# Kernel optimization log

Hardware: AMD Instinct MI355X
Metric: run time of the kernel (lower is better)

Reference implementation:

```python
import jax, jax.numpy as jnp
import numpy as np

B, K, IN_DIM, H, D = 8, 4096, 512, 8, 64  # batch, tokens, in_dim, heads, per-head dim


def setup_inputs() -> dict:
    key = jax.random.key(0)
    ks = jax.random.split(key, 8)
    s = 0.02
    return {
        "x": jax.random.normal(ks[0], (B, K, IN_DIM), jnp.float32),
        "y": jax.random.normal(ks[1], (B, K, IN_DIM), jnp.float32),
        "Wq": jax.random.normal(ks[2], (IN_DIM, H * D), jnp.float32) * s,
        "bq": jnp.zeros((H * D,), jnp.float32),
        "Wk": jax.random.normal(ks[3], (IN_DIM, H * D), jnp.float32) * s,
        "bk": jnp.zeros((H * D,), jnp.float32),
        "Wv": jax.random.normal(ks[4], (IN_DIM, H * D), jnp.float32) * s,
        "bv": jnp.zeros((H * D,), jnp.float32),
        "Wp": jax.random.normal(ks[5], (IN_DIM, D), jnp.float32) * s,
        "gamma": jax.random.uniform(ks[6], (H, 1, 1, 1), jnp.float32) + 0.001,
    }


def _heads(t):
    # (B, K, H*D) -> (H, B, K, D); matches split_cat(t, D, dim=2, cat dim=0) head-major layout
    b, k, _ = t.shape
    return t.reshape(b, k, H, D).transpose(2, 0, 1, 3)


def reference(x, y, Wq, bq, Wk, bk, Wv, bv, Wp, gamma):
    q = _heads(x @ Wq + bq)   # (H,B,K,D)
    kk = _heads(x @ Wk + bk)  # (H,B,K,D)
    v = _heads(y @ Wv + bv)   # (H,B,K,D)
    # energy = q^T k contracted over tokens -> (H,B,D,D)
    energy = jnp.einsum('hbkd,hbke->hbde', q, kk)
    attn = jax.nn.softmax(energy, axis=-1)
    # out = v @ attn^T : out[k,q] = sum_e v[k,e] * attn[q,e]
    out = jnp.einsum('hbke,hbqe->hbkq', v, attn)  # (H,B,K,D)
    yp = y @ Wp  # projection(y): (B,K,D)
    out = (gamma * out + yp[None]) / (1.0 + gamma)
    return out.transpose(1, 0, 2, 3)  # (B,H,K,D)
```

## Files before the change

### kernel.cpp

```cpp
#include <hip/hip_runtime.h>

#define B_ 8
#define K_ 4096
#define IN_ 512
#define H_ 8
#define D_ 64
#define HD_ 512

typedef short bf16x8 __attribute__((ext_vector_type(8)));
typedef float f32x4 __attribute__((ext_vector_type(4)));
typedef unsigned short u16;
typedef unsigned short us8v __attribute__((ext_vector_type(8)));
typedef unsigned short us4v __attribute__((ext_vector_type(4)));

__device__ inline u16 f2bf_rn(float f) {
  unsigned u = __float_as_uint(f);
  u += 0x7fffu + ((u >> 16) & 1u);
  return (u16)(u >> 16);
}
__device__ inline float bf2f(u16 h) {
  return __uint_as_float(((unsigned)h) << 16);
}

__device__ inline void gl_lds16(const u16* g, u16* l) {
  __builtin_amdgcn_global_load_lds(
      (const __attribute__((address_space(1))) unsigned int*)g,
      (__attribute__((address_space(3))) unsigned int*)l, 16, 0, 0);
}


__global__ __launch_bounds__(256) void k_cvt_x(const float* __restrict__ x,
                                               u16* __restrict__ xt_hi,
                                               u16* __restrict__ xt_lo,
                                               float* __restrict__ svec) {
  const int kt = blockIdx.x, ct = blockIdx.y, b = blockIdx.z;
  __shared__ float Xs[64][65];
  const int tid = threadIdx.x;
  const float* src = x + ((size_t)b * K_ + kt * 64) * IN_ + ct * 64;
#pragma unroll
  for (int r = 0; r < 4; ++r) {
    int idx = tid + 256 * r;
    int k = idx >> 4, c4 = (idx & 15) * 4;
    f32x4 v = *(const f32x4*)(src + (size_t)k * IN_ + c4);
    Xs[k][c4 + 0] = v[0];
    Xs[k][c4 + 1] = v[1];
    Xs[k][c4 + 2] = v[2];
    Xs[k][c4 + 3] = v[3];
  }
  __syncthreads();
  if (tid < 64) {
    float s = 0.f;
#pragma unroll
    for (int k = 0; k < 64; ++k) s += Xs[k][tid];
    atomicAdd(&svec[b * IN_ + ct * 64 + tid], s);
  }
#pragma unroll
  for (int r = 0; r < 2; ++r) {
    int idx = tid + 256 * r;
    int c = idx >> 3, ck = (idx & 7) * 8;
    us8v hv, lv;
#pragma unroll
    for (int j = 0; j < 8; ++j) {
      float f = Xs[ck + j][c];
      u16 h = f2bf_rn(f);
      float lo = f - bf2f(h);
      hv[j] = h;
      lv[j] = f2bf_rn(lo);
    }
    size_t off = ((size_t)(b * IN_ + ct * 64 + c)) * K_ + kt * 64 + ck;
    *(us8v*)(xt_hi + off) = hv;
    *(us8v*)(xt_lo + off) = lv;
  }
}

__global__ __launch_bounds__(256) void k_cvt_y(const float* __restrict__ y,
                                               u16* __restrict__ yb) {
  size_t i = ((size_t)blockIdx.x * 256 + threadIdx.x) * 8;
  f32x4 v0 = *(const f32x4*)(y + i);
  f32x4 v1 = *(const f32x4*)(y + i + 4);
  us8v o;
  o[0] = f2bf_rn(v0[0]); o[1] = f2bf_rn(v0[1]);
  o[2] = f2bf_rn(v0[2]); o[3] = f2bf_rn(v0[3]);
  o[4] = f2bf_rn(v1[0]); o[5] = f2bf_rn(v1[1]);
  o[6] = f2bf_rn(v1[2]); o[7] = f2bf_rn(v1[3]);
  *(us8v*)(yb + i) = o;
}

__global__ __launch_bounds__(256) void k_cvt_w(
    const float* __restrict__ Wq, const float* __restrict__ Wk,
    u16* __restrict__ Wqt_hi, u16* __restrict__ Wqt_lo,
    u16* __restrict__ Wkt_hi, u16* __restrict__ Wkt_lo) {
  const int ti = blockIdx.x, tj = blockIdx.y;
  const float* src = blockIdx.z ? Wk : Wq;
  u16* dhi = blockIdx.z ? Wkt_hi : Wqt_hi;
  u16* dlo = blockIdx.z ? Wkt_lo : Wqt_lo;
  __shared__ float T[64][65];
  const int tid = threadIdx.x;
#pragma unroll
  for (int r = 0; r < 4; ++r) {
    int idx = tid + 256 * r;
    int rr = idx >> 4, c4 = (idx & 15) * 4;
    f32x4 v = *(const f32x4*)(src + (size_t)(tj * 64 + rr) * 512 + ti * 64 + c4);
    T[rr][c4 + 0] = v[0]; T[rr][c4 + 1] = v[1];
    T[rr][c4 + 2] = v[2]; T[rr][c4 + 3] = v[3];
  }
  __syncthreads();
#pragma unroll
  for (int r = 0; r < 2; ++r) {
    int idx = tid + 256 * r;
    int d = idx >> 3, ck = (idx & 7) * 8;
    us8v hv, lv;
#pragma unroll
    for (int j = 0; j < 8; ++j) {
      float f = T[ck + j][d];
      u16 h = f2bf_rn(f);
      hv[j] = h;
      lv[j] = f2bf_rn(f - bf2f(h));
    }
    size_t off = (size_t)(ti * 64 + d) * 512 + tj * 64 + ck;
    *(us8v*)(dhi + off) = hv;
    *(us8v*)(dlo + off) = lv;
  }
}

#define GP 72

__global__ __launch_bounds__(256, 2) void k_gram_mfma(
    const u16* __restrict__ xt_hi, const u16* __restrict__ xt_lo,
    float* __restrict__ G) {
  const int fid = blockIdx.x;
  const int kc = fid & 7;
  const int slot = fid >> 3;
  const int b = slot / 10;
  int pp = slot - b * 10, ti = 0;
  while (pp >= 4 - ti) { pp -= 4 - ti; ++ti; }
  const int tj = ti + pp;
  const bool diag = (ti == tj);
  __shared__ u16 P[4 * 128 * 64];
  u16* Pih = P;
  u16* Pil = P + 128 * 64;
  u16* Pjh = P + 2 * 128 * 64;
  u16* Pjl = P + 3 * 128 * 64;
  const int tid = threadIdx.x;
  const int wave = tid >> 6, lane = tid & 63;
  const int wm = wave & 1, wn = wave >> 1;
  const int m16 = lane & 15, quad = lane >> 4;
  const size_t base_i = ((size_t)(b * IN_ + ti * 128)) * K_;
  const size_t base_j = ((size_t)(b * IN_ + tj * 128)) * K_;
  const int lrow = lane >> 3;
  const int lcol = ((lane & 7) * 8) ^ (lrow << 3);
  const size_t loff = (size_t)lrow * K_ + lcol;
  const u16* PBh = diag ? Pih : Pjh;
  const u16* PBl = diag ? Pil : Pjl;

  f32x4 zf = {0.f, 0.f, 0.f, 0.f};
  f32x4 acc[4][4];
#pragma unroll
  for (int mt = 0; mt < 4; ++mt)
#pragma unroll
    for (int nt = 0; nt < 4; ++nt) acc[mt][nt] = zf;
  const int kbeg = kc * 512, kend = kbeg + 512;

  for (int k0 = kbeg; k0 < kend; k0 += 64) {
    __syncthreads();
#pragma unroll
    for (int r = 0; r < 4; ++r) {
      int rg = wave * 4 + r;
      size_t go = (size_t)(rg * 8) * K_ + k0 + loff;
      int lo = rg * 8 * 64;
      gl_lds16(xt_hi + base_i + go, &Pih[lo]);
      gl_lds16(xt_lo + base_i + go, &Pil[lo]);
      if (!diag) {
        gl_lds16(xt_hi + base_j + go, &Pjh[lo]);
        gl_lds16(xt_lo + base_j + go, &Pjl[lo]);
      }
    }
    __syncthreads();
#pragma unroll
    for (int kk = 0; kk < 64; kk += 32) {
      const int ac = (kk + quad * 8) ^ ((m16 & 7) << 3);
      bf16x8 ah[4], al[4], bh[4], bl[4];
#pragma unroll
      for (int t = 0; t < 4; ++t) {
        int ar = (wm * 64 + t * 16 + m16) * 64 + ac;
        ah[t] = *(const bf16x8*)&Pih[ar];
        al[t] = *(const bf16x8*)&Pil[ar];
        int br = (wn * 64 + t * 16 + m16) * 64 + ac;
        bh[t] = *(const bf16x8*)&PBh[br];
        bl[t] = *(const bf16x8*)&PBl[br];
      }
#pragma unroll
      for (int mt = 0; mt < 4; ++mt)
#pragma unroll
        for (int nt = 0; nt < 4; ++nt) {
          acc[mt][nt] = __builtin_amdgcn_mfma_f32_16x16x32_bf16(
              ah[mt], bh[nt], acc[mt][nt], 0, 0, 0);
          acc[mt][nt] = __builtin_amdgcn_mfma_f32_16x16x32_bf16(
              ah[mt], bl[nt], acc[mt][nt], 0, 0, 0);
          acc[mt][nt] = __builtin_amdgcn_mfma_f32_16x16x32_bf16(
              al[mt], bh[nt], acc[mt][nt], 0, 0, 0);
        }
    }
  }
  float* Gb = G + (size_t)b * IN_ * IN_;
#pragma unroll
  for (int mt = 0; mt < 4; ++mt)
#pragma unroll
    for (int nt = 0; nt < 4; ++nt)
#pragma unroll
      for (int r = 0; r < 4; ++r) {
        int gi = ti * 128 + wm * 64 + mt * 16 + quad * 4 + r;
        int gj = tj * 128 + wn * 64 + nt * 16 + m16;
        atomicAdd(&Gb[(size_t)gi * IN_ + gj], acc[mt][nt][r]);
      }
}

__global__ __launch_bounds__(256) void k_cvt_g(const float* __restrict__ G,
                                               u16* __restrict__ Ghi,
                                               u16* __restrict__ Glo) {
  const int ti = blockIdx.x, tj = blockIdx.y, b = blockIdx.z;
  if (tj < ti) return;
  const float* Gb = G + (size_t)b * IN_ * IN_;
  u16* ghb = Ghi + (size_t)b * IN_ * IN_;
  u16* glb = Glo + (size_t)b * IN_ * IN_;
  __shared__ float T[64][65];
  const int tid = threadIdx.x;
#pragma unroll
  for (int r = 0; r < 4; ++r) {
    int idx = tid + 256 * r;
    int rr = idx >> 4, c4 = (idx & 15) * 4;
    f32x4 v = *(const f32x4*)(Gb + (size_t)(ti * 64 + rr) * IN_ + tj * 64 + c4);
    T[rr][c4 + 0] = v[0]; T[rr][c4 + 1] = v[1];
    T[rr][c4 + 2] = v[2]; T[rr][c4 + 3] = v[3];
  }
  __syncthreads();
#pragma unroll
  for (int r = 0; r < 2; ++r) {
    int idx = tid + 256 * r;
    int rr = idx >> 3, ck = (idx & 7) * 8;
    us8v hv, lv;
#pragma unroll
    for (int j = 0; j < 8; ++j) {
      float f = T[rr][ck + j];
      u16 h = f2bf_rn(f);
      hv[j] = h;
      lv[j] = f2bf_rn(f - bf2f(h));
    }
    size_t off = (size_t)(ti * 64 + rr) * IN_ + tj * 64 + ck;
    *(us8v*)(ghb + off) = hv;
    *(us8v*)(glb + off) = lv;
  }
  if (ti != tj) {
#pragma unroll
    for (int r = 0; r < 2; ++r) {
      int idx = tid + 256 * r;
      int rr = idx >> 3, ck = (idx & 7) * 8;
      us8v hv, lv;
#pragma unroll
      for (int j = 0; j < 8; ++j) {
        float f = T[ck + j][rr];
        u16 h = f2bf_rn(f);
        hv[j] = h;
        lv[j] = f2bf_rn(f - bf2f(h));
      }
      size_t off = (size_t)(tj * 64 + rr) * IN_ + ti * 64 + ck;
      *(us8v*)(ghb + off) = hv;
      *(us8v*)(glb + off) = lv;
    }
  }
}

__global__ __launch_bounds__(256) void k_aall_mfma(
    const u16* __restrict__ Wqt_hi, const u16* __restrict__ Wqt_lo,
    const u16* __restrict__ Ghi, const u16* __restrict__ Glo,
    u16* __restrict__ Ahi, u16* __restrict__ Alo) {
  const int ct = blockIdx.x;
  const int hb = blockIdx.y;
  const int h = hb >> 3, b = hb & 7;
  __shared__ u16 S[4 * 64 * 64];
  u16* Ah = S;
  u16* Al = S + 64 * 64;
  u16* Bh = S + 2 * 64 * 64;
  u16* Bl = S + 3 * 64 * 64;
  const int tid = threadIdx.x;
  const int wave = tid >> 6, lane = tid & 63;
  const int m16 = lane & 15, quad = lane >> 4;
  const u16* Abase_h = Wqt_hi + (size_t)(h * 64) * IN_;
  const u16* Abase_l = Wqt_lo + (size_t)(h * 64) * IN_;
  const u16* Bbase_h = Ghi + (size_t)b * IN_ * IN_ + (size_t)(ct * 64) * IN_;
  const u16* Bbase_l = Glo + (size_t)b * IN_ * IN_ + (size_t)(ct * 64) * IN_;
  const int lrow = lane >> 3;
  const int lcol = ((lane & 7) * 8) ^ (lrow << 3);
  const size_t loff = (size_t)lrow * IN_ + lcol;
  f32x4 zf = {0.f, 0.f, 0.f, 0.f};
  f32x4 acc[4] = {zf, zf, zf, zf};
  for (int k0 = 0; k0 < IN_; k0 += 64) {
    __syncthreads();
#pragma unroll
    for (int r = 0; r < 2; ++r) {
      int rg = wave * 2 + r;
      size_t go = (size_t)(rg * 8) * IN_ + k0 + loff;
      int lo = rg * 8 * 64;
      gl_lds16(Abase_h + go, &Ah[lo]);
      gl_lds16(Abase_l + go, &Al[lo]);
      gl_lds16(Bbase_h + go, &Bh[lo]);
      gl_lds16(Bbase_l + go, &Bl[lo]);
    }
    __syncthreads();
#pragma unroll
    for (int kk = 0; kk < 64; kk += 32) {
      const int ac = (kk + quad * 8) ^ ((m16 & 7) << 3);
      int arow = (wave * 16 + m16) * 64 + ac;
      bf16x8 ah = *(const bf16x8*)&Ah[arow];
      bf16x8 al = *(const bf16x8*)&Al[arow];
#pragma unroll
      for (int n = 0; n < 4; ++n) {
        int brow = (n * 16 + m16) * 64 + ac;
        bf16x8 bh = *(const bf16x8*)&Bh[brow];
        bf16x8 bl = *(const bf16x8*)&Bl[brow];
        acc[n] = __builtin_amdgcn_mfma_f32_16x16x32_bf16(ah, bh, acc[n], 0, 0, 0);
        acc[n] = __builtin_amdgcn_mfma_f32_16x16x32_bf16(ah, bl, acc[n], 0, 0, 0);
        acc[n] = __builtin_amdgcn_mfma_f32_16x16x32_bf16(al, bh, acc[n], 0, 0, 0);
      }
    }
  }
  __syncthreads();
  float* Sf = (float*)S;
#pragma unroll
  for (int n = 0; n < 4; ++n)
#pragma unroll
    for (int r = 0; r < 4; ++r) {
      int d = wave * 16 + quad * 4 + r;
      int cc = n * 16 + m16;
      Sf[d * 68 + cc] = acc[n][r];
    }
  __syncthreads();
#pragma unroll
  for (int r = 0; r < 2; ++r) {
    int idx = tid + 256 * r;
    int d = idx >> 3, ck = (idx & 7) * 8;
    us8v hv, lv;
#pragma unroll
    for (int j = 0; j < 8; ++j) {
      float f = Sf[d * 68 + ck + j];
      u16 h2 = f2bf_rn(f);
      hv[j] = h2;
      lv[j] = f2bf_rn(f - bf2f(h2));
    }
    size_t off = ((size_t)hb * 64 + d) * IN_ + ct * 64 + ck;
    *(us8v*)(Ahi + off) = hv;
    *(us8v*)(Alo + off) = lv;
  }
}

__global__ __launch_bounds__(256) void k_attn3(
    const u16* __restrict__ Ahi, const u16* __restrict__ Alo,
    const u16* __restrict__ Wqt_hi, const u16* __restrict__ Wqt_lo,
    const u16* __restrict__ Wkt_hi, const u16* __restrict__ Wkt_lo,
    const float* __restrict__ Wv, const float* __restrict__ Wp,
    const float* __restrict__ bq, const float* __restrict__ bk,
    const float* __restrict__ bv, const float* __restrict__ gamma,
    const float* __restrict__ svec, u16* __restrict__ Wft,
    float* __restrict__ bfin) {
  const int h = blockIdx.x, b = blockIdx.y;
  const int hb = h * B_ + b;
  const int tid = threadIdx.x;
  const int wave = tid >> 6, lane = tid & 63;
  const int m16 = lane & 15, quad = lane >> 4;
  __shared__ u16 S[4 * 64 * GP];
  __shared__ float Esh[64][65];
  __shared__ float t1[64], t2[64];
  u16* Ah = S;
  u16* Al = S + 64 * GP;
  u16* Bh = S + 2 * 64 * GP;
  u16* Bl = S + 3 * 64 * GP;

  if (tid < 64) {
    float s = 0.f;
    const u16* wh = Wkt_hi + (size_t)(h * 64 + tid) * IN_;
    const u16* wl = Wkt_lo + (size_t)(h * 64 + tid) * IN_;
    const float* sv = svec + b * IN_;
    for (int c = 0; c < IN_; c += 8) {
      us8v hv = *(const us8v*)(wh + c);
      us8v lv = *(const us8v*)(wl + c);
#pragma unroll
      for (int j = 0; j < 8; ++j)
        s += sv[c + j] * (bf2f(hv[j]) + bf2f(lv[j]));
    }
    t1[tid] = s;
  } else if (tid < 128) {
    int d = tid - 64;
    float s = 0.f;
    const u16* wh = Wqt_hi + (size_t)(h * 64 + d) * IN_;
    const u16* wl = Wqt_lo + (size_t)(h * 64 + d) * IN_;
    const float* sv = svec + b * IN_;
    for (int c = 0; c < IN_; c += 8) {
      us8v hv = *(const us8v*)(wh + c);
      us8v lv = *(const us8v*)(wl + c);
#pragma unroll
      for (int j = 0; j < 8; ++j)
        s += sv[c + j] * (bf2f(hv[j]) + bf2f(lv[j]));
    }
    t2[d] = s;
  }

  const u16* Abase_h = Ahi + (size_t)hb * 64 * IN_;
  const u16* Abase_l = Alo + (size_t)hb * 64 * IN_;
  const u16* Bbase_h = Wkt_hi + (size_t)(h * 64) * IN_;
  const u16* Bbase_l = Wkt_lo + (size_t)(h * 64) * IN_;
  f32x4 zf = {0.f, 0.f, 0.f, 0.f};
  f32x4 acc[4] = {zf, zf, zf, zf};
  for (int k0 = 0; k0 < IN_; k0 += 64) {
    __syncthreads();
#pragma unroll
    for (int r = 0; r < 2; ++r) {
      int idx = tid + 256 * r;
      int row = idx >> 3, ck = (idx & 7) * 8;
      int lo = row * GP + ck;
      *(us8v*)&Ah[lo] = *(const us8v*)(Abase_h + (size_t)row * IN_ + k0 + ck);
      *(us8v*)&Al[lo] = *(const us8v*)(Abase_l + (size_t)row * IN_ + k0 + ck);
      *(us8v*)&Bh[lo] = *(const us8v*)(Bbase_h + (size_t)row * IN_ + k0 + ck);
      *(us8v*)&Bl[lo] = *(const us8v*)(Bbase_l + (size_t)row * IN_ + k0 + ck);
    }
    __syncthreads();
#pragma unroll
    for (int kk = 0; kk < 64; kk += 32) {
      int arow = (wave * 16 + m16) * GP + kk + quad * 8;
      bf16x8 ah = *(const bf16x8*)&Ah[arow];
      bf16x8 al = *(const bf16x8*)&Al[arow];
#pragma unroll
      for (int n = 0; n < 4; ++n) {
        int brow = (n * 16 + m16) * GP + kk + quad * 8;
        bf16x8 bh = *(const bf16x8*)&Bh[brow];
        bf16x8 bl = *(const bf16x8*)&Bl[brow];
        acc[n] = __builtin_amdgcn_mfma_f32_16x16x32_bf16(ah, bh, acc[n], 0, 0, 0);
        acc[n] = __builtin_amdgcn_mfma_f32_16x16x32_bf16(ah, bl, acc[n], 0, 0, 0);
        acc[n] = __builtin_amdgcn_mfma_f32_16x16x32_bf16(al, bh, acc[n], 0, 0, 0);
      }
    }
  }
  __syncthreads();
#pragma unroll
  for (int n = 0; n < 4; ++n)
#pragma unroll
    for (int r = 0; r < 4; ++r) {
      int d = wave * 16 + quad * 4 + r;
      int e = n * 16 + m16;
      float bqd = bq[h * D_ + d], bke = bk[h * D_ + e];
      Esh[d][e] = acc[n][r] + bqd * t1[e] + t2[d] * bke + (float)K_ * bqd * bke;
    }
  __syncthreads();
  const float g = gamma[h];
  const float inv1g = 1.f / (1.f + g);
  if (tid < 64) {
    float m = -1e30f;
    for (int e = 0; e < 64; ++e) m = fmaxf(m, Esh[tid][e]);
    float ssum = 0.f;
    for (int e = 0; e < 64; ++e) {
      float p = __expf(Esh[tid][e] - m);
      Esh[tid][e] = p;
      ssum += p;
    }
    float inv = 1.f / ssum;
    float bsum = 0.f;
    for (int e = 0; e < 64; ++e) {
      Esh[tid][e] *= inv;
      bsum += bv[h * D_ + e] * Esh[tid][e];
    }
    bfin[hb * D_ + tid] = g * bsum * inv1g;
  }
  __syncthreads();

  bf16x8 bfr[4][2];
#pragma unroll
  for (int n = 0; n < 4; ++n)
#pragma unroll
    for (int kk = 0; kk < 2; ++kk)
#pragma unroll
      for (int j = 0; j < 8; ++j)
        bfr[n][kk][j] = f2bf_rn(Esh[n * 16 + m16][kk * 32 + quad * 8 + j]);

  u16* Wf = Wft + (size_t)hb * D_ * IN_;
#pragma unroll
  for (int mt = 0; mt < 8; ++mt) {
    f32x4 a4[4] = {zf, zf, zf, zf};
#pragma unroll
    for (int kk = 0; kk < 2; ++kk) {
      int c = wave * 128 + mt * 16 + m16;
      const float* wv = Wv + (size_t)c * HD_ + h * D_ + kk * 32 + quad * 8;
      f32x4 v0 = *(const f32x4*)wv;
      f32x4 v1 = *(const f32x4*)(wv + 4);
      bf16x8 af;
      af[0] = f2bf_rn(v0[0]); af[1] = f2bf_rn(v0[1]);
      af[2] = f2bf_rn(v0[2]); af[3] = f2bf_rn(v0[3]);
      af[4] = f2bf_rn(v1[0]); af[5] = f2bf_rn(v1[1]);
      af[6] = f2bf_rn(v1[2]); af[7] = f2bf_rn(v1[3]);
#pragma unroll
      for (int n = 0; n < 4; ++n)
        a4[n] = __builtin_amdgcn_mfma_f32_16x16x32_bf16(af, bfr[n][kk], a4[n], 0, 0, 0);
    }
    int cb = wave * 128 + mt * 16 + quad * 4;
#pragma unroll
    for (int n = 0; n < 4; ++n) {
      int q = n * 16 + m16;
      us4v st;
#pragma unroll
      for (int r = 0; r < 4; ++r) {
        float val = (g * a4[n][r] + Wp[(size_t)(cb + r) * D_ + q]) * inv1g;
        st[r] = f2bf_rn(val);
      }
      *(us4v*)(Wf + (size_t)q * IN_ + cb) = st;
    }
  }
}

__global__ __launch_bounds__(256, 2) void k_out_mfma(
    const u16* __restrict__ yb, const u16* __restrict__ Wft,
    const float* __restrict__ bfin, float* __restrict__ out) {
  const int kt = blockIdx.x;
  const int b = blockIdx.y & 7, hq = blockIdx.y >> 3;
  const int h0 = hq * 2;
  __shared__ u16 Wsh[2][2 * 64 * 64];
  const int tid = threadIdx.x, wave = tid >> 6, lane = tid & 63;
  const int m16 = lane & 15, quad = lane >> 4;
  const int swz = (m16 & 7) << 3;

  us8v stg[4];
  auto LOAD = [&](int c0) {
#pragma unroll
    for (int r = 0; r < 4; ++r) {
      int idx = tid + 256 * r;
      int row = idx >> 3, ck = (idx & 7) * 8;
      int i = row >> 6, q = row & 63;
      const u16* src =
          Wft + ((size_t)((h0 + i) * 8 + b) * 64 + q) * IN_ + c0 + ck;
      stg[r] = *(const us8v*)src;
    }
  };
  auto WRITE = [&](int buf) {
#pragma unroll
    for (int r = 0; r < 4; ++r) {
      int idx = tid + 256 * r;
      int row = idx >> 3, ck = (idx & 7) * 8;
      *(us8v*)&Wsh[buf][row * 64 + (ck ^ ((row & 7) << 3))] = stg[r];
    }
  };
  bf16x8 yf[2][4];
  auto LOADY = [&](bf16x8 (*yd)[4], int c0) {
#pragma unroll
    for (int kk = 0; kk < 2; ++kk)
#pragma unroll
      for (int ms = 0; ms < 4; ++ms) {
        int row = kt * 256 + wave * 64 + ms * 16 + m16;
        yd[kk][ms] = *(const bf16x8*)(yb + ((size_t)b * K_ + row) * IN_ + c0 +
                                      kk * 32 + quad * 8);
      }
  };

  f32x4 zf = {0.f, 0.f, 0.f, 0.f};
  f32x4 acc[4][2][4];
#pragma unroll
  for (int ms = 0; ms < 4; ++ms)
#pragma unroll
    for (int i = 0; i < 2; ++i)
#pragma unroll
      for (int nt = 0; nt < 4; ++nt) acc[ms][i][nt] = zf;

  LOAD(0);
  LOADY(yf, 0);
  WRITE(0);
  __syncthreads();
  int cur = 0;
  for (int c0 = 0; c0 < IN_; c0 += 64) {
    const bool more = (c0 + 64 < IN_);
    bf16x8 yn[2][4];
    if (more) {
      LOAD(c0 + 64);
      LOADY(yn, c0 + 64);
    }
#pragma unroll
    for (int kk = 0; kk < 2; ++kk)
#pragma unroll
      for (int i = 0; i < 2; ++i)
#pragma unroll
        for (int nt = 0; nt < 4; ++nt) {
          int brow = i * 64 + nt * 16 + m16;
          bf16x8 bb = *(const bf16x8*)&Wsh[cur][brow * 64 +
                                               ((kk * 32 + quad * 8) ^ swz)];
#pragma unroll
          for (int ms = 0; ms < 4; ++ms)
            acc[ms][i][nt] = __builtin_amdgcn_mfma_f32_16x16x32_bf16(
                yf[kk][ms], bb, acc[ms][i][nt], 0, 0, 0);
        }
    if (more) {
      WRITE(cur ^ 1);
      __syncthreads();
      cur ^= 1;
#pragma unroll
      for (int kk = 0; kk < 2; ++kk)
#pragma unroll
        for (int ms = 0; ms < 4; ++ms) yf[kk][ms] = yn[kk][ms];
    }
  }

#pragma unroll
  for (int i = 0; i < 2; ++i) {
    float* ob = out + (((size_t)b * H_ + h0 + i) * K_) * D_;
    const int hb = (h0 + i) * 8 + b;
#pragma unroll
    for (int ms = 0; ms < 4; ++ms)
#pragma unroll
      for (int nt = 0; nt < 4; ++nt) {
        int col = nt * 16 + m16;
        float bf = bfin[hb * D_ + col];
#pragma unroll
        for (int r = 0; r < 4; ++r) {
          int row = kt * 256 + wave * 64 + ms * 16 + quad * 4 + r;
          ob[(size_t)row * D_ + col] = acc[ms][i][nt][r] + bf;
        }
      }
  }
}

__global__ __launch_bounds__(256) void k_gram(const float* __restrict__ x,
                                              float* __restrict__ G,
                                              float* __restrict__ svec) {
  const int it = blockIdx.x, jt = blockIdx.y, b = blockIdx.z;
  if (jt < it) return;
  __shared__ float Xi[16][64];
  __shared__ float Xj[16][64];
  const float* Xb = x + (size_t)b * K_ * IN_;
  const int tx = threadIdx.x, ty = threadIdx.y;
  const int tid = ty * 16 + tx;
  const int i0 = it * 64, j0 = jt * 64;
  const bool diag = (it == jt);
  float acc[4][4] = {};
  float ssum = 0.f;
  for (int k0 = 0; k0 < K_; k0 += 16) {
#pragma unroll
    for (int r = 0; r < 4; ++r) {
      int idx = tid + 256 * r;
      int kk = idx >> 6, cc = idx & 63;
      const float* row = Xb + (size_t)(k0 + kk) * IN_;
      Xi[kk][cc] = row[i0 + cc];
      Xj[kk][cc] = row[j0 + cc];
    }
    __syncthreads();
#pragma unroll
    for (int kk = 0; kk < 16; ++kk) {
      float a[4], bb[4];
#pragma unroll
      for (int u = 0; u < 4; ++u) a[u] = Xi[kk][ty * 4 + u];
#pragma unroll
      for (int u = 0; u < 4; ++u) bb[u] = Xj[kk][tx * 4 + u];
#pragma unroll
      for (int u = 0; u < 4; ++u)
#pragma unroll
        for (int w = 0; w < 4; ++w) acc[u][w] += a[u] * bb[w];
    }
    if (diag && tid < 64) {
#pragma unroll
      for (int kk = 0; kk < 16; ++kk) ssum += Xi[kk][tid];
    }
    __syncthreads();
  }
  float* Gb = G + (size_t)b * IN_ * IN_;
#pragma unroll
  for (int u = 0; u < 4; ++u)
#pragma unroll
    for (int w = 0; w < 4; ++w) {
      int gi = i0 + ty * 4 + u, gj = j0 + tx * 4 + w;
      Gb[(size_t)gi * IN_ + gj] = acc[u][w];
      if (!diag) Gb[(size_t)gj * IN_ + gi] = acc[u][w];
    }
  if (diag && tid < 64) svec[b * IN_ + i0 + tid] = ssum;
}

__global__ __launch_bounds__(256) void k_aall(const float* __restrict__ Wq,
                                              const float* __restrict__ G,
                                              float* __restrict__ Aall) {
  const int jt = blockIdx.x;
  const int h = blockIdx.y, b = blockIdx.z;
  __shared__ float Ws[16][64];
  __shared__ float Gs[16][64];
  const float* Gb = G + (size_t)b * IN_ * IN_;
  const int tx = threadIdx.x, ty = threadIdx.y;
  const int tid = ty * 16 + tx;
  float acc[4][4] = {};
  for (int c0 = 0; c0 < IN_; c0 += 16) {
#pragma unroll
    for (int r = 0; r < 4; ++r) {
      int idx = tid + 256 * r;
      int kk = idx >> 6, cc = idx & 63;
      Ws[kk][cc] = Wq[(size_t)(c0 + kk) * HD_ + h * D_ + cc];
      Gs[kk][cc] = Gb[(size_t)(c0 + kk) * IN_ + jt * 64 + cc];
    }
    __syncthreads();
#pragma unroll
    for (int kk = 0; kk < 16; ++kk) {
      float a[4], bb[4];
#pragma unroll
      for (int u = 0; u < 4; ++u) a[u] = Ws[kk][ty * 4 + u];
#pragma unroll
      for (int u = 0; u < 4; ++u) bb[u] = Gs[kk][tx * 4 + u];
#pragma unroll
      for (int u = 0; u < 4; ++u)
#pragma unroll
        for (int w = 0; w < 4; ++w) acc[u][w] += a[u] * bb[w];
    }
    __syncthreads();
  }
  const int hb = h * B_ + b;
  float* Ahb = Aall + (size_t)hb * D_ * IN_;
#pragma unroll
  for (int u = 0; u < 4; ++u)
#pragma unroll
    for (int w = 0; w < 4; ++w)
      Ahb[(size_t)(ty * 4 + u) * IN_ + jt * 64 + tx * 4 + w] = acc[u][w];
}

__global__ __launch_bounds__(256) void k_attn_f32(
    const float* __restrict__ Wq, const float* __restrict__ Wk,
    const float* __restrict__ Wv, const float* __restrict__ Wp,
    const float* __restrict__ bq, const float* __restrict__ bk,
    const float* __restrict__ bv, const float* __restrict__ gamma,
    const float* __restrict__ Aall, const float* __restrict__ svec,
    float* __restrict__ Wfin, float* __restrict__ bfin) {
  const int h = blockIdx.x, b = blockIdx.y;
  const int hb = h * B_ + b;
  const int tx = threadIdx.x, ty = threadIdx.y;
  const int tid = ty * 16 + tx;
  __shared__ float Ast[64][17];
  __shared__ float Ws[16][64];
  __shared__ float Esh[64][65];
  __shared__ float t1[64], t2[64];
  const float* Ahb = Aall + (size_t)hb * D_ * IN_;
  if (tid < 64) {
    float a2 = 0.f;
    for (int c = 0; c < IN_; ++c)
      a2 += svec[b * IN_ + c] * Wk[(size_t)c * HD_ + h * D_ + tid];
    t1[tid] = a2;
  } else if (tid < 128) {
    int d = tid - 64;
    float a2 = 0.f;
    for (int c = 0; c < IN_; ++c)
      a2 += svec[b * IN_ + c] * Wq[(size_t)c * HD_ + h * D_ + d];
    t2[d] = a2;
  }
  float acc[4][4] = {};
  for (int c0 = 0; c0 < IN_; c0 += 16) {
#pragma unroll
    for (int r = 0; r < 4; ++r) {
      int idx = tid + 256 * r;
      int dd = idx >> 4, kk = idx & 15;
      Ast[dd][kk] = Ahb[(size_t)dd * IN_ + c0 + kk];
      int kk2 = idx >> 6, ee = idx & 63;
      Ws[kk2][ee] = Wk[(size_t)(c0 + kk2) * HD_ + h * D_ + ee];
    }
    __syncthreads();
#pragma unroll
    for (int kk = 0; kk < 16; ++kk) {
      float a[4], bb[4];
#pragma unroll
      for (int u = 0; u < 4; ++u) a[u] = Ast[ty * 4 + u][kk];
#pragma unroll
      for (int u = 0; u < 4; ++u) bb[u] = Ws[kk][tx * 4 + u];
#pragma unroll
      for (int u = 0; u < 4; ++u)
#pragma unroll
        for (int w = 0; w < 4; ++w) acc[u][w] += a[u] * bb[w];
    }
    __syncthreads();
  }
#pragma unroll
  for (int u = 0; u < 4; ++u) {
    int d = ty * 4 + u;
    float bqd = bq[h * D_ + d];
    float t2d = t2[d];
#pragma unroll
    for (int w = 0; w < 4; ++w) {
      int e = tx * 4 + w;
      float bke = bk[h * D_ + e];
      Esh[d][e] = acc[u][w] + bqd * t1[e] + t2d * bke + (float)K_ * bqd * bke;
    }
  }
  __syncthreads();
  if (tid < 64) {
    float m = -1e30f;
    for (int e = 0; e < 64; ++e) m = fmaxf(m, Esh[tid][e]);
    float ssum = 0.f;
    for (int e = 0; e < 64; ++e) {
      float p = __expf(Esh[tid][e] - m);
      Esh[tid][e] = p;
      ssum += p;
    }
    float inv = 1.f / ssum;
    for (int e = 0; e < 64; ++e) Esh[tid][e] *= inv;
  }
  __syncthreads();
  const float g = gamma[h];
  const float inv1g = 1.f / (1.f + g);
  if (tid < 64) {
    float a2 = 0.f;
    for (int e = 0; e < 64; ++e) a2 += bv[h * D_ + e] * Esh[tid][e];
    bfin[hb * D_ + tid] = g * a2 * inv1g;
  }
  float* Wf = Wfin + (size_t)hb * IN_ * D_;
  for (int it2 = 0; it2 < 128; ++it2) {
    int idx = tid + 256 * it2;
    int c = idx >> 6, q = idx & 63;
    const float* Wvr = Wv + (size_t)c * HD_ + h * D_;
    float a2 = 0.f;
#pragma unroll
    for (int e = 0; e < 64; ++e) a2 += Wvr[e] * Esh[q][e];
    Wf[idx] = (g * a2 + Wp[(size_t)c * D_ + q]) * inv1g;
  }
}

__global__ __launch_bounds__(256) void k_out_f32(const float* __restrict__ y,
                                                 const float* __restrict__ Wfin,
                                                 const float* __restrict__ bfin,
                                                 float* __restrict__ out) {
  const int kt = blockIdx.x;
  const int hb = blockIdx.y;
  const int h = hb >> 3, b = hb & 7;
  __shared__ float Ys[64][17];
  __shared__ float Ws[16][64];
  const int tx = threadIdx.x, ty = threadIdx.y;
  const int tid = ty * 16 + tx;
  const float* Yb = y + (size_t)b * K_ * IN_;
  const float* Wf = Wfin + (size_t)hb * IN_ * D_;
  const int k0 = kt * 64;
  float acc[4][4] = {};
  for (int c0 = 0; c0 < IN_; c0 += 16) {
#pragma unroll
    for (int r = 0; r < 4; ++r) {
      int idx = tid + 256 * r;
      int rr = idx >> 4, kk = idx & 15;
      Ys[rr][kk] = Yb[(size_t)(k0 + rr) * IN_ + c0 + kk];
      int kk2 = idx >> 6, qq = idx & 63;
      Ws[kk2][qq] = Wf[(size_t)(c0 + kk2) * D_ + qq];
    }
    __syncthreads();
#pragma unroll
    for (int kk = 0; kk < 16; ++kk) {
      float a[4], bb[4];
#pragma unroll
      for (int u = 0; u < 4; ++u) a[u] = Ys[ty * 4 + u][kk];
#pragma unroll
      for (int u = 0; u < 4; ++u) bb[u] = Ws[kk][tx * 4 + u];
#pragma unroll
      for (int u = 0; u < 4; ++u)
#pragma unroll
        for (int w = 0; w < 4; ++w) acc[u][w] += a[u] * bb[w];
    }
    __syncthreads();
  }
  float* ob = out + (((size_t)b * H_ + h) * K_ + k0) * D_;
#pragma unroll
  for (int u = 0; u < 4; ++u) {
    int k = ty * 4 + u;
#pragma unroll
    for (int w = 0; w < 4; ++w) {
      int q = tx * 4 + w;
      ob[(size_t)k * D_ + q] = acc[u][w] + bfin[hb * D_ + q];
    }
  }
}

extern "C" void kernel_launch(void* const* d_in, const int* in_sizes, int n_in,
                              void* d_out, int out_size, void* d_ws,
                              size_t ws_size, hipStream_t stream) {
  const float* x = (const float*)d_in[0];
  const float* y = (const float*)d_in[1];
  const float* Wq = (const float*)d_in[2];
  const float* bq = (const float*)d_in[3];
  const float* Wk = (const float*)d_in[4];
  const float* bk = (const float*)d_in[5];
  const float* Wv = (const float*)d_in[6];
  const float* bv = (const float*)d_in[7];
  const float* Wp = (const float*)d_in[8];
  const float* gm = (const float*)d_in[9];
  float* out = (float*)d_out;

  const size_t NEED = 86016000;
  if (ws_size >= NEED) {
    char* w = (char*)d_ws;
    u16* xt_hi = (u16*)(w);
    u16* Ahi = (u16*)(w);
    u16* Alo = (u16*)(w + 4194304);
    u16* Wft = (u16*)(w + 8388608);
    u16* xt_lo = (u16*)(w + 33554432);
    u16* yb = (u16*)(w + 33554432);
    float* G = (float*)(w + 67108864);
    u16* Ghi = (u16*)(w + 75497472);
    u16* Glo = (u16*)(w + 79691776);
    u16* Wqt_hi = (u16*)(w + 83886080);
    u16* Wqt_lo = (u16*)(w + 84410368);
    u16* Wkt_hi = (u16*)(w + 84934656);
    u16* Wkt_lo = (u16*)(w + 85458944);
    float* bfin = (float*)(w + 85983232);
    float* svec = (float*)(w + 85999616);

    hipMemsetAsync(G, 0, 8388608, stream);
    hipMemsetAsync(svec, 0, 16384, stream);
    k_cvt_w<<<dim3(8, 8, 2), 256, 0, stream>>>(Wq, Wk, Wqt_hi, Wqt_lo, Wkt_hi,
                                               Wkt_lo);
    k_cvt_x<<<dim3(64, 8, 8), 256, 0, stream>>>(x, xt_hi, xt_lo, svec);
    k_gram_mfma<<<dim3(640), 256, 0, stream>>>(xt_hi, xt_lo, G);
    k_cvt_y<<<dim3(8192), 256, 0, stream>>>(y, yb);
    k_cvt_g<<<dim3(8, 8, 8), 256, 0, stream>>>(G, Ghi, Glo);
    k_aall_mfma<<<dim3(8, 64), 256, 0, stream>>>(Wqt_hi, Wqt_lo, Ghi, Glo, Ahi,
                                                 Alo);
    k_attn3<<<dim3(8, 8), 256, 0, stream>>>(Ahi, Alo, Wqt_hi, Wqt_lo, Wkt_hi,
                                            Wkt_lo, Wv, Wp, bq, bk, bv, gm,
                                            svec, Wft, bfin);
    k_out_mfma<<<dim3(16, 32), 256, 0, stream>>>(yb, Wft, bfin, out);
  } else {
    float* ws = (float*)d_ws;
    float* G = ws;
    float* Aall = ws + 2097152;
    float* Wfin = ws + 4194304;
    float* bfin = ws + 6291456;
    float* svec = ws + 6295552;
    dim3 blk(16, 16);
    k_gram<<<dim3(8, 8, 8), blk, 0, stream>>>(x, G, svec);
    k_aall<<<dim3(8, 8, 8), blk, 0, stream>>>(Wq, G, Aall);
    k_attn_f32<<<dim3(8, 8), blk, 0, stream>>>(Wq, Wk, Wv, Wp, bq, bk, bv, gm,
                                               Aall, svec, Wfin, bfin);
    k_out_f32<<<dim3(64, 64), blk, 0, stream>>>(y, Wfin, bfin, out);
  }
}
```

Measured before the change: 332.4 us.

## Double-buffer LDS staging in gram MFMA kernel with 32-wide k steps

Restructures the gram kernel's main loop to prefetch the next 32-column k-slice into a second LDS buffer while MFMAs run on the current one. Step size drops from 64 to 32 with a new XOR swizzle for the narrower rows, and total LDS stays the same. This removes one barrier per iteration and aims to overlap global-to-LDS loads with compute. The cost is twice as many loop iterations and barriers relative to work, and more correctness risk from the new swizzle.

```diff
diff --git a/kernel.cpp b/kernel.cpp
--- a/kernel.cpp
+++ b/kernel.cpp
@@ -136,22 +136,16 @@
   while (pp >= 4 - ti) { pp -= 4 - ti; ++ti; }
   const int tj = ti + pp;
   const bool diag = (ti == tj);
-  __shared__ u16 P[4 * 128 * 64];
-  u16* Pih = P;
-  u16* Pil = P + 128 * 64;
-  u16* Pjh = P + 2 * 128 * 64;
-  u16* Pjl = P + 3 * 128 * 64;
+  __shared__ u16 P[2][4 * 128 * 32];
   const int tid = threadIdx.x;
   const int wave = tid >> 6, lane = tid & 63;
   const int wm = wave & 1, wn = wave >> 1;
   const int m16 = lane & 15, quad = lane >> 4;
   const size_t base_i = ((size_t)(b * IN_ + ti * 128)) * K_;
   const size_t base_j = ((size_t)(b * IN_ + tj * 128)) * K_;
-  const int lrow = lane >> 3;
-  const int lcol = ((lane & 7) * 8) ^ (lrow << 3);
-  const size_t loff = (size_t)lrow * K_ + lcol;
-  const u16* PBh = diag ? Pih : Pjh;
-  const u16* PBl = diag ? Pil : Pjl;
+  const int sr = lane >> 2, sslot = lane & 3;
+  const int boff_h = diag ? 0 : 2 * 4096;
+  const int boff_l = diag ? 4096 : 3 * 4096;
 
   f32x4 zf = {0.f, 0.f, 0.f, 0.f};
   f32x4 acc[4][4];
@@ -159,48 +153,56 @@
   for (int mt = 0; mt < 4; ++mt)
 #pragma unroll
     for (int nt = 0; nt < 4; ++nt) acc[mt][nt] = zf;
-  const int kbeg = kc * 512, kend = kbeg + 512;
-
-  for (int k0 = kbeg; k0 < kend; k0 += 64) {
-    __syncthreads();
-#pragma unroll
-    for (int r = 0; r < 4; ++r) {
-      int rg = wave * 4 + r;
-      size_t go = (size_t)(rg * 8) * K_ + k0 + loff;
-      int lo = rg * 8 * 64;
-      gl_lds16(xt_hi + base_i + go, &Pih[lo]);
-      gl_lds16(xt_lo + base_i + go, &Pil[lo]);
+  const int kbeg = kc * 512;
+
+  auto STAGE = [&](int t, int buf) {
+    const int k0 = kbeg + t * 32;
+    u16* Pb = &P[buf][0];
+#pragma unroll
+    for (int g = 0; g < 2; ++g) {
+      int rbase = wave * 32 + g * 16;
+      int r = rbase + sr;
+      size_t go = (size_t)r * K_ + k0 + ((sslot ^ (r & 3)) << 3);
+      int lo = rbase * 32;
+      gl_lds16(xt_hi + base_i + go, Pb + 0 * 4096 + lo);
+      gl_lds16(xt_lo + base_i + go, Pb + 1 * 4096 + lo);
       if (!diag) {
-        gl_lds16(xt_hi + base_j + go, &Pjh[lo]);
-        gl_lds16(xt_lo + base_j + go, &Pjl[lo]);
+        gl_lds16(xt_hi + base_j + go, Pb + 2 * 4096 + lo);
+        gl_lds16(xt_lo + base_j + go, Pb + 3 * 4096 + lo);
       }
     }
-    __syncthreads();
-#pragma unroll
-    for (int kk = 0; kk < 64; kk += 32) {
-      const int ac = (kk + quad * 8) ^ ((m16 & 7) << 3);
-      bf16x8 ah[4], al[4], bh[4], bl[4];
-#pragma unroll
-      for (int t = 0; t < 4; ++t) {
-        int ar = (wm * 64 + t * 16 + m16) * 64 + ac;
-        ah[t] = *(const bf16x8*)&Pih[ar];
-        al[t] = *(const bf16x8*)&Pil[ar];
-        int br = (wn * 64 + t * 16 + m16) * 64 + ac;
-        bh[t] = *(const bf16x8*)&PBh[br];
-        bl[t] = *(const bf16x8*)&PBl[br];
+  };
+
+  STAGE(0, 0);
+  __syncthreads();
+  int cur = 0;
+  const int ac = ((quad ^ (m16 & 3)) << 3);
+  for (int t = 0; t < 16; ++t) {
+    if (t < 15) STAGE(t + 1, cur ^ 1);
+    const u16* Pb = &P[cur][0];
+    bf16x8 ah[4], al[4], bh[4], bl[4];
+#pragma unroll
+    for (int tt = 0; tt < 4; ++tt) {
+      int ar = (wm * 64 + tt * 16 + m16) * 32 + ac;
+      ah[tt] = *(const bf16x8*)(Pb + ar);
+      al[tt] = *(const bf16x8*)(Pb + 4096 + ar);
+      int br = (wn * 64 + tt * 16 + m16) * 32 + ac;
+      bh[tt] = *(const bf16x8*)(Pb + boff_h + br);
+      bl[tt] = *(const bf16x8*)(Pb + boff_l + br);
+    }
+#pragma unroll
+    for (int mt = 0; mt < 4; ++mt)
+#pragma unroll
+      for (int nt = 0; nt < 4; ++nt) {
+        acc[mt][nt] = __builtin_amdgcn_mfma_f32_16x16x32_bf16(
+            ah[mt], bh[nt], acc[mt][nt], 0, 0, 0);
+        acc[mt][nt] = __builtin_amdgcn_mfma_f32_16x16x32_bf16(
+            ah[mt], bl[nt], acc[mt][nt], 0, 0, 0);
+        acc[mt][nt] = __builtin_amdgcn_mfma_f32_16x16x32_bf16(
+            al[mt], bh[nt], acc[mt][nt], 0, 0, 0);
       }
-#pragma unroll
-      for (int mt = 0; mt < 4; ++mt)
-#pragma unroll
-        for (int nt = 0; nt < 4; ++nt) {
-          acc[mt][nt] = __builtin_amdgcn_mfma_f32_16x16x32_bf16(
-              ah[mt], bh[nt], acc[mt][nt], 0, 0, 0);
-          acc[mt][nt] = __builtin_amdgcn_mfma_f32_16x16x32_bf16(
-              ah[mt], bl[nt], acc[mt][nt], 0, 0, 0);
-          acc[mt][nt] = __builtin_amdgcn_mfma_f32_16x16x32_bf16(
-              al[mt], bh[nt], acc[mt][nt], 0, 0, 0);
-        }
-    }
+    __syncthreads();
+    cur ^= 1;
   }
   float* Gb = G + (size_t)b * IN_ * IN_;
 #pragma unroll
```

New measurement: 334.1 us. No clear change (+0.5%).
